# Optimization experiments

Hardware: AMD Instinct MI355X
Metric: run time of the kernel (lower is better)

Reference implementation:

```python
import jax, jax.numpy as jnp
import numpy as np

N = 1024          # number of junctions
H = 1024          # heatmap height
W = 1024          # heatmap width
NUM_SAMPLES = 64  # samples along each candidate segment (torch_sampler)
DETECT_THRESH = 0.5
INLIER_THRESH = 0.99


def setup_inputs() -> dict:
    key = jax.random.key(0)
    k1, k2 = jax.random.split(key)
    # junctions are (h, w) float coordinates inside the image
    junctions = jax.random.uniform(k1, (N, 2), dtype=jnp.float32) * (H - 1)
    heatmap = jax.random.uniform(k2, (H, W), dtype=jnp.float32)
    return {"junctions": junctions, "heatmap": heatmap}


def _bilinear_sample(heatmap, ch, cw):
    """SOLD2 detect_bilinear: gather 4 corners, bilinear weights. ch/cw: [N,N,S]."""
    hf = jnp.floor(ch); hc = jnp.ceil(ch)
    wf = jnp.floor(cw); wc = jnp.ceil(cw)
    hfi = hf.astype(jnp.int32); hci = hc.astype(jnp.int32)
    wfi = wf.astype(jnp.int32); wci = wc.astype(jnp.int32)
    return (heatmap[hfi, wfi] * (hc - ch) * (wc - cw)
          + heatmap[hfi, wci] * (hc - ch) * (cw - wf)
          + heatmap[hci, wfi] * (ch - hf) * (wc - cw)
          + heatmap[hci, wci] * (ch - hf) * (cw - wf))


def reference(junctions, heatmap):
    n = junctions.shape[0]
    Hh, Ww = heatmap.shape
    t = jnp.linspace(0.0, 1.0, NUM_SAMPLES, dtype=jnp.float32)  # [S]
    # cand_samples[i, j, s] = junc[i] * t[s] + junc[j] * (1 - t[s])  (start=i, end=j)
    ch = junctions[:, None, 0:1] * t + junctions[None, :, 0:1] * (1.0 - t)  # [N,N,S]
    cw = junctions[:, None, 1:2] * t + junctions[None, :, 1:2] * (1.0 - t)  # [N,N,S]
    ch = jnp.clip(ch, 0.0, Hh - 1)
    cw = jnp.clip(cw, 0.0, Ww - 1)
    feat = _bilinear_sample(heatmap, ch, cw)                    # [N,N,S]
    mean_feat = feat.mean(axis=-1)                              # [N,N]
    inlier_ratio = (feat > DETECT_THRESH).astype(jnp.float32).mean(axis=-1)
    # candidate map: strict upper triangle (torch.triu(ones, diagonal=1))
    cand_mask = jnp.triu(jnp.ones((n, n), dtype=bool), k=1)
    detected = (mean_feat > DETECT_THRESH) & (inlier_ratio >= INLIER_THRESH) & cand_mask
    line_map = (detected | detected.T).astype(jnp.int32)        # symmetric line map
    return line_map, mean_feat
```

## Files before the change

kernel.cpp:

```cpp
#include <hip/hip_runtime.h>

#define NJ 1024
#define DETECT 0.5f
#define RESCUE 0.4975f

__global__ __launch_bounds__(256) void pack_kernel(
    const float* __restrict__ heat, unsigned int* __restrict__ packed)
{
    const int idx = blockIdx.x * 256 + threadIdx.x;
    const int h = idx >> 10;
    const int w = idx & 1023;
    const int hn = (h < 1023) ? h + 1 : 1023;
    const int wn = (w < 1023) ? w + 1 : 1023;
    const float* r0 = heat + (h  << 10);
    const float* r1 = heat + (hn << 10);
    const unsigned int b0 = (unsigned int)__float2int_rn(r0[w]  * 255.0f);
    const unsigned int b1 = (unsigned int)__float2int_rn(r0[wn] * 255.0f);
    const unsigned int b2 = (unsigned int)__float2int_rn(r1[w]  * 255.0f);
    const unsigned int b3 = (unsigned int)__float2int_rn(r1[wn] * 255.0f);
    packed[idx] = b0 | (b1 << 8) | (b2 << 16) | (b3 << 24);
}

__device__ __forceinline__ float sample_t(int s) {
    return (s == 63) ? 1.0f : (float)s * (1.0f / 63.0f);
}

__global__ __launch_bounds__(256) void sold2_thread_kernel(
    const float* __restrict__ junc,
    const float* __restrict__ heat,
    const unsigned int* __restrict__ packed,
    float* __restrict__ line_out,
    float* __restrict__ mean_out)
{
    const int q = blockIdx.x * 256 + threadIdx.x;
    const int r = q / 513;
    const int c = q - r * 513;
    const int j = (r + c) & 1023;

    const float2 jr  = ((const float2*)junc)[r];
    const float2 jjc = ((const float2*)junc)[j];

    float acc = 0.0f;
    float mn  = __builtin_inff();

    #pragma unroll
    for (int s0 = 0; s0 < 64; s0 += 16) {
        float chv[16], cwv[16];
        unsigned int cv[16];
        #pragma unroll
        for (int u = 0; u < 16; ++u) {
            const int s = s0 + u;
            const float t  = sample_t(s);
            const float om = 1.0f - t;
            float ch = __fadd_rn(__fmul_rn(jr.x, t), __fmul_rn(jjc.x, om));
            float cw = __fadd_rn(__fmul_rn(jr.y, t), __fmul_rn(jjc.y, om));
            ch = fminf(fmaxf(ch, 0.0f), 1023.0f);
            cw = fminf(fmaxf(cw, 0.0f), 1023.0f);
            chv[u] = ch;
            cwv[u] = cw;
            const int hfi = (int)ch;
            const int wfi = (int)cw;
            cv[u] = packed[(hfi << 10) + wfi];
        }
        #pragma unroll
        for (int u = 0; u < 16; ++u) {
            const float ch = chv[u], cw = cwv[u];
            const float hf = floorf(ch), hc = ceilf(ch);
            const float wf = floorf(cw), wc = ceilf(cw);
            const float wh0 = hc - ch, wh1 = ch - hf;
            const float ww0 = wc - cw, ww1 = cw - wf;
            const unsigned int cc = cv[u];
            const float a00 = (float)(cc & 0xffu);
            const float a01 = (float)((cc >> 8) & 0xffu);
            const float a10 = (float)((cc >> 16) & 0xffu);
            const float a11 = (float)(cc >> 24);
            const float feat = a00 * (wh0 * ww0) + a01 * (wh0 * ww1)
                             + a10 * (wh1 * ww0) + a11 * (wh1 * ww1);
            acc += feat;
            mn = fminf(mn, feat);
        }
    }

    float mean = acc * (1.0f / (255.0f * 64.0f));
    const float mns = mn * (1.0f / 255.0f);

    bool det = false;
    if ((mns > RESCUE) && (mean > RESCUE) && (c != 0)) {
        float acc2 = 0.0f;
        float mn2  = __builtin_inff();
        for (int s = 0; s < 64; ++s) {
            const float t  = sample_t(s);
            const float om = 1.0f - t;
            float ch = __fadd_rn(__fmul_rn(jr.x, t), __fmul_rn(jjc.x, om));
            float cw = __fadd_rn(__fmul_rn(jr.y, t), __fmul_rn(jjc.y, om));
            ch = fminf(fmaxf(ch, 0.0f), 1023.0f);
            cw = fminf(fmaxf(cw, 0.0f), 1023.0f);
            const float hf = floorf(ch), hc = ceilf(ch);
            const float wf = floorf(cw), wc = ceilf(cw);
            const int hfi = (int)hf, hci = (int)hc;
            const int wfi = (int)wf, wci = (int)wc;
            const float a00 = heat[(hfi << 10) + wfi];
            const float a01 = heat[(hfi << 10) + wci];
            const float a10 = heat[(hci << 10) + wfi];
            const float a11 = heat[(hci << 10) + wci];
            const float t1 = __fmul_rn(__fmul_rn(a00, __fsub_rn(hc, ch)), __fsub_rn(wc, cw));
            const float t2 = __fmul_rn(__fmul_rn(a01, __fsub_rn(hc, ch)), __fsub_rn(cw, wf));
            const float t3 = __fmul_rn(__fmul_rn(a10, __fsub_rn(ch, hf)), __fsub_rn(wc, cw));
            const float t4 = __fmul_rn(__fmul_rn(a11, __fsub_rn(ch, hf)), __fsub_rn(cw, wf));
            const float feat = __fadd_rn(__fadd_rn(__fadd_rn(t1, t2), t3), t4);
            acc2 += feat;
            mn2 = fminf(mn2, feat);
        }
        mean = acc2 * (1.0f / 64.0f);
        det = (mean > DETECT) && (mn2 > DETECT);
    }

    const float lv = det ? 1.0f : 0.0f;
    const int p1 = (r << 10) + j;
    const int p2 = (j << 10) + r;
    mean_out[p1] = mean;
    mean_out[p2] = mean;
    line_out[p1] = lv;
    line_out[p2] = lv;
}

extern "C" void kernel_launch(void* const* d_in, const int* in_sizes, int n_in,
                              void* d_out, int out_size, void* d_ws, size_t ws_size,
                              hipStream_t stream) {
    const float* junc = (const float*)d_in[0];
    const float* heat = (const float*)d_in[1];
    float* line_out = (float*)d_out;
    float* mean_out = line_out + NJ * NJ;

    unsigned int* packed = (unsigned int*)d_ws;
    pack_kernel<<<NJ * NJ / 256, 256, 0, stream>>>(heat, packed);

    const int total = NJ * 513;
    sold2_thread_kernel<<<total / 256, 256, 0, stream>>>(junc, heat, packed,
                                                         line_out, mean_out);
}
```

Baseline: 191.6 us.

## Vectorize heatmap packing and move transposed mirror writes to tiled kernel

The pack kernel now processes four columns per thread using float4 loads and a uint4 store, cutting the thread count and load instructions. The main kernel writes only the direct (r, j) entry. A new mirror kernel, using shared-memory 64x64 tiles, fills the symmetric half and replaces the uncoalesced scattered transposed stores. In exchange, the outputs are read and written again in an extra launch.

```diff
diff --git a/kernel.cpp b/kernel.cpp
--- a/kernel.cpp
+++ b/kernel.cpp
@@ -5,20 +5,32 @@
 #define RESCUE 0.4975f
 
 __global__ __launch_bounds__(256) void pack_kernel(
-    const float* __restrict__ heat, unsigned int* __restrict__ packed)
+    const float* __restrict__ heat, uint4* __restrict__ packed4)
 {
     const int idx = blockIdx.x * 256 + threadIdx.x;
-    const int h = idx >> 10;
-    const int w = idx & 1023;
+    const int h = idx >> 8;
+    const int w4 = (idx & 255) << 2;
     const int hn = (h < 1023) ? h + 1 : 1023;
-    const int wn = (w < 1023) ? w + 1 : 1023;
     const float* r0 = heat + (h  << 10);
     const float* r1 = heat + (hn << 10);
-    const unsigned int b0 = (unsigned int)__float2int_rn(r0[w]  * 255.0f);
-    const unsigned int b1 = (unsigned int)__float2int_rn(r0[wn] * 255.0f);
-    const unsigned int b2 = (unsigned int)__float2int_rn(r1[w]  * 255.0f);
-    const unsigned int b3 = (unsigned int)__float2int_rn(r1[wn] * 255.0f);
-    packed[idx] = b0 | (b1 << 8) | (b2 << 16) | (b3 << 24);
+    const float4 a = *(const float4*)(r0 + w4);
+    const float4 b = *(const float4*)(r1 + w4);
+    const int wnext = (w4 + 4 <= 1023) ? w4 + 4 : 1023;
+    const float a4 = r0[wnext];
+    const float b4 = r1[wnext];
+
+    const float av[5] = {a.x, a.y, a.z, a.w, a4};
+    const float bv[5] = {b.x, b.y, b.z, b.w, b4};
+    unsigned int out[4];
+    #pragma unroll
+    for (int u = 0; u < 4; ++u) {
+        const unsigned int c0 = (unsigned int)__float2int_rn(av[u]     * 255.0f);
+        const unsigned int c1 = (unsigned int)__float2int_rn(av[u + 1] * 255.0f);
+        const unsigned int c2 = (unsigned int)__float2int_rn(bv[u]     * 255.0f);
+        const unsigned int c3 = (unsigned int)__float2int_rn(bv[u + 1] * 255.0f);
+        out[u] = c0 | (c1 << 8) | (c2 << 16) | (c3 << 24);
+    }
+    packed4[idx] = make_uint4(out[0], out[1], out[2], out[3]);
 }
 
 __device__ __forceinline__ float sample_t(int s) {
@@ -115,13 +127,42 @@
         det = (mean > DETECT) && (mn2 > DETECT);
     }
 
-    const float lv = det ? 1.0f : 0.0f;
     const int p1 = (r << 10) + j;
-    const int p2 = (j << 10) + r;
     mean_out[p1] = mean;
-    mean_out[p2] = mean;
-    line_out[p1] = lv;
-    line_out[p2] = lv;
+    line_out[p1] = det ? 1.0f : 0.0f;
+}
+
+__global__ __launch_bounds__(256) void mirror_kernel(
+    float* __restrict__ line_out, float* __restrict__ mean_out)
+{
+    __shared__ float lm[64][65];
+    __shared__ float mm[64][65];
+    const int bi = blockIdx.x >> 4;
+    const int bj = blockIdx.x & 15;
+    const int tx = threadIdx.x & 63;
+    const int g  = threadIdx.x >> 6;
+
+    #pragma unroll
+    for (int k = 0; k < 16; ++k) {
+        const int b = (g << 4) + k;
+        const int src = ((bj << 6) + b) * 1024 + (bi << 6) + tx;
+        lm[b][tx] = line_out[src];
+        mm[b][tx] = mean_out[src];
+    }
+    __syncthreads();
+
+    #pragma unroll
+    for (int k = 0; k < 16; ++k) {
+        const int a = (g << 4) + k;
+        const int i = (bi << 6) + a;
+        const int j = (bj << 6) + tx;
+        const int d = (j - i) & 1023;
+        if (d >= 513) {
+            const int dst = i * 1024 + j;
+            line_out[dst] = lm[tx][a];
+            mean_out[dst] = mm[tx][a];
+        }
+    }
 }
 
 extern "C" void kernel_launch(void* const* d_in, const int* in_sizes, int n_in,
@@ -133,9 +174,11 @@
     float* mean_out = line_out + NJ * NJ;
 
     unsigned int* packed = (unsigned int*)d_ws;
-    pack_kernel<<<NJ * NJ / 256, 256, 0, stream>>>(heat, packed);
+    pack_kernel<<<1024, 256, 0, stream>>>(heat, (uint4*)packed);
 
     const int total = NJ * 513;
     sold2_thread_kernel<<<total / 256, 256, 0, stream>>>(junc, heat, packed,
                                                          line_out, mean_out);
+
+    mirror_kernel<<<256, 256, 0, stream>>>(line_out, mean_out);
 }
```

After: 188.2 us. No clear change (-1.8%).
